# Performance work log

Hardware: AMD Instinct MI355X
Metric: run time of the kernel (lower is better)

## Reference

```python
import jax, jax.numpy as jnp
import numpy as np

N_LAYERS = 200
KSIZE = 7
L_IN = 1388
FC_IN = 188   # 1388 - 200*6
FC_OUT = 91


def setup_inputs() -> dict:
    key = jax.random.key(0)
    k_x, k_w, k_b, k_fw, k_fb = jax.random.split(key, 5)
    B = 1024
    x = jax.random.normal(k_x, (B, L_IN), dtype=jnp.float32)
    # Conv1d(1,1,7) weights: torch default init U(-s, s) with s = 1/sqrt(in_ch*k) = 1/sqrt(7)
    s = 1.0 / np.sqrt(KSIZE)
    conv_w = jax.random.uniform(k_w, (N_LAYERS, KSIZE), dtype=jnp.float32, minval=-s, maxval=s)
    conv_b = jax.random.uniform(k_b, (N_LAYERS,), dtype=jnp.float32, minval=-s, maxval=s)
    sf = 1.0 / np.sqrt(FC_IN)
    fc_w = jax.random.uniform(k_fw, (FC_OUT, FC_IN), dtype=jnp.float32, minval=-sf, maxval=sf)
    fc_b = jax.random.uniform(k_fb, (FC_OUT,), dtype=jnp.float32, minval=-sf, maxval=sf)
    return {"x": x, "conv_w": conv_w, "conv_b": conv_b, "fc_w": fc_w, "fc_b": fc_b}


def _conv1(h, w, b):
    # h: [B, L]; cross-correlation with taps w[0..6], valid padding -> [B, L-6]
    L_out = h.shape[1] - (KSIZE - 1)
    acc = w[0] * h[:, 0:L_out]
    for k in range(1, KSIZE):
        acc = acc + w[k] * h[:, k:k + L_out]
    return acc + b


def reference(x, conv_w, conv_b, fc_w, fc_b):
    h = x  # unsqueeze(1) is implicit: single channel handled as [B, L]
    for i in range(N_LAYERS):
        h = _conv1(h, conv_w[i], conv_b[i])
        if i < N_LAYERS - 1:  # last ReLU was popped in the torch module
            h = jax.nn.relu(h)
    # Linear(188, 91) applied to the length dim, then Sigmoid; squeeze channel dim
    out = jax.nn.sigmoid(h @ fc_w.T + fc_b)  # [B, 91]
    return out
```

## Files before the change

kernel.cpp:

```cpp
#include <hip/hip_runtime.h>
#include <math.h>

#define N_LAYERS 200
#define KSIZE 7
#define L_IN 1388
#define FC_IN 188
#define FC_OUT 91
#define NT 128
#define RMAX 13


template<int R, bool RELU>
__device__ __forceinline__ void run_stage(float (&r)[RMAX], float (&h)[6],
                                          const float* __restrict__ cw,
                                          const float* __restrict__ cb,
                                          int i0, int i1)
{
    constexpr int S = (R < 6) ? R : 6;
    float w[KSIZE], b;
#pragma unroll
    for (int d = 0; d < KSIZE; ++d) w[d] = cw[i0 * KSIZE + d];
    b = cb[i0];

#pragma unroll 1
    for (int i = i0; i < i1; ++i) {
#pragma unroll
        for (int k = 0; k < S; ++k) {
            float acc = b;
#pragma unroll
            for (int d = 0; d < KSIZE; ++d) {
                const int m = k + d;
                const float v = (m < R) ? r[m] : h[m - R];
                acc = fmaf(w[d], v, acc);
            }
            r[k] = RELU ? fmaxf(acc, 0.0f) : acc;
        }

        float hn[6];
#pragma unroll
        for (int t = 0; t < 6; ++t)
            hn[t] = __shfl_down(r[t % R], 1 + t / R);

        float w2[KSIZE], b2;
        const int ip = (i + 1 < i1) ? (i + 1) : i;
#pragma unroll
        for (int d = 0; d < KSIZE; ++d) w2[d] = cw[ip * KSIZE + d];
        b2 = cb[ip];

#pragma unroll
        for (int k = S; k < R; ++k) {
            float acc = b;
#pragma unroll
            for (int d = 0; d < KSIZE; ++d) {
                const int m = k + d;
                const float v = (m < R) ? r[m] : h[m - R];
                acc = fmaf(w[d], v, acc);
            }
            r[k] = RELU ? fmaxf(acc, 0.0f) : acc;
        }

#pragma unroll
        for (int t = 0; t < 6; ++t) h[t] = hn[t];
#pragma unroll
        for (int d = 0; d < KSIZE; ++d) w[d] = w2[d];
        b = b2;
    }
}

template<int Ro, int Rn>
__device__ __forceinline__ void repack(float (&r)[RMAX], float (&h)[6],
                                       float* lbuf, int lane,
                                       int base_o, int bound, int base_n)
{
#pragma unroll
    for (int k = 0; k < Ro; ++k) {
        const int g = base_o + lane * Ro + k;
        if (g < bound) lbuf[g] = r[k];
    }
    __syncthreads();
#pragma unroll
    for (int k = 0; k < Rn; ++k) r[k] = lbuf[base_n + lane * Rn + k];
#pragma unroll
    for (int t = 0; t < 6; ++t) h[t] = lbuf[base_n + lane * Rn + Rn + t];
    __syncthreads();
}

__global__ __launch_bounds__(NT) void conv_chain_kernel(
    const float* __restrict__ x,
    const float* __restrict__ conv_w,
    const float* __restrict__ conv_b,
    const float* __restrict__ fc_w,
    const float* __restrict__ fc_b,
    float* __restrict__ out)
{
    __shared__ __align__(16) float lbuf[1216];

    const int row  = blockIdx.x;
    const int tid  = threadIdx.x;
    const int lane = tid & 63;
    const int wid  = tid >> 6;

    float r[RMAX], h[6];
    const float* xr = x + (size_t)row * L_IN;
    const int base0 = wid ? 598 : 0;
#pragma unroll
    for (int k = 0; k < 13; ++k) {
        const int p = base0 + lane * 13 + k;
        r[k] = (p < L_IN) ? xr[p] : 0.0f;
    }
#pragma unroll
    for (int t = 0; t < 6; ++t) {
        const int p = base0 + lane * 13 + 13 + t;
        h[t] = (p < L_IN) ? xr[p] : 0.0f;
    }

    run_stage<13, true>(r, h, conv_w, conv_b,   0,  32);
    repack<13, 11>(r, h, lbuf, lane, wid ? 598 : 0, wid ? 1196 : 598, wid ? 502 : 0);
    run_stage<11, true>(r, h, conv_w, conv_b,  32,  64);
    repack<11, 10>(r, h, lbuf, lane, wid ? 502 : 0, wid ? 1004 : 502, wid ? 406 : 0);
    run_stage<10, true>(r, h, conv_w, conv_b,  64,  96);
    repack<10,  8>(r, h, lbuf, lane, wid ? 406 : 0, wid ?  812 : 406, wid ? 310 : 0);
    run_stage< 8, true>(r, h, conv_w, conv_b,  96, 128);
    repack< 8,  7>(r, h, lbuf, lane, wid ? 310 : 0, wid ?  620 : 310, wid ? 214 : 0);
    run_stage< 7, true>(r, h, conv_w, conv_b, 128, 160);
    repack< 7,  5>(r, h, lbuf, lane, wid ? 214 : 0, wid ?  428 : 214, wid ? 118 : 0);
    run_stage< 5, true>(r, h, conv_w, conv_b, 160, 192);
    repack< 5,  3>(r, h, lbuf, lane, wid ? 118 : 0, wid ?  236 : 118, wid ?  94 : 0);
    run_stage< 3, true >(r, h, conv_w, conv_b, 192, 199);
    run_stage< 3, false>(r, h, conv_w, conv_b, 199, 200);

    {
        const int bo = wid ? 94 : 0;
        const int bd = wid ? 188 : 94;
#pragma unroll
        for (int k = 0; k < 3; ++k) {
            const int g = bo + lane * 3 + k;
            if (g < bd) lbuf[g] = r[k];
        }
    }
    __syncthreads();

    if (tid < FC_OUT) {
        float acc = fc_b[tid];
        const float4* wp = (const float4*)(fc_w + tid * FC_IN);
        const float4* hp = (const float4*)lbuf;
#pragma unroll 4
        for (int q = 0; q < FC_IN / 4; ++q) {
            const float4 hv = hp[q];
            const float4 wv = wp[q];
            acc = fmaf(wv.x, hv.x, acc);
            acc = fmaf(wv.y, hv.y, acc);
            acc = fmaf(wv.z, hv.z, acc);
            acc = fmaf(wv.w, hv.w, acc);
        }
        out[(size_t)row * FC_OUT + tid] = 1.0f / (1.0f + expf(-acc));
    }
}

extern "C" void kernel_launch(void* const* d_in, const int* in_sizes, int n_in,
                              void* d_out, int out_size, void* d_ws, size_t ws_size,
                              hipStream_t stream) {
    const float* x      = (const float*)d_in[0];
    const float* conv_w = (const float*)d_in[1];
    const float* conv_b = (const float*)d_in[2];
    const float* fc_w   = (const float*)d_in[3];
    const float* fc_b   = (const float*)d_in[4];
    float* outp = (float*)d_out;

    const int batch = in_sizes[0] / L_IN;
    conv_chain_kernel<<<batch, NT, 0, stream>>>(x, conv_w, conv_b, fc_w, fc_b, outp);
}
```

Baseline: 135.7 us.

## Split conv chain across four waves with frequent LDS repacks

Doubles the block to four wavefronts per row, so each lane holds at most six outputs instead of thirteen. Repacking through shared memory now happens every eight layers, across 25 compile-time stages, instead of every 32. This shortens each thread's serial per-layer work and lowers register pressure, but adds many more barriers and LDS round trips, and the 1024-block grid now uses more threads per block.

```diff
diff --git a/kernel.cpp b/kernel.cpp
--- a/kernel.cpp
+++ b/kernel.cpp
@@ -6,9 +6,18 @@
 #define L_IN 1388
 #define FC_IN 188
 #define FC_OUT 91
-#define NT 128
-#define RMAX 13
+#define NT 256
+#define NW 4
+#define RMAX 6
+#define NSTAGES 25
 
+constexpr int len_end(int s) { return 1340 - 48 * s; }
+constexpr int stage_R(int s) {
+    const int l = len_end(s);
+    const int q = l / 4;
+    const int own3 = l - 3 * q;
+    return (own3 + 48 + 63) / 64;
+}
 
 template<int R, bool RELU>
 __device__ __forceinline__ void run_stage(float (&r)[RMAX], float (&h)[6],
@@ -69,21 +78,62 @@
 
 template<int Ro, int Rn>
 __device__ __forceinline__ void repack(float (&r)[RMAX], float (&h)[6],
-                                       float* lbuf, int lane,
-                                       int base_o, int bound, int base_n)
+                                       float* lbuf, int lane, int wid,
+                                       int len1, int q1, int q2)
 {
+    const int base_o = wid * q1;
+    const int bound  = (wid == 3) ? len1 : base_o + q1;
 #pragma unroll
     for (int k = 0; k < Ro; ++k) {
         const int g = base_o + lane * Ro + k;
         if (g < bound) lbuf[g] = r[k];
     }
     __syncthreads();
+    const int base_n = wid * q2;
 #pragma unroll
     for (int k = 0; k < Rn; ++k) r[k] = lbuf[base_n + lane * Rn + k];
 #pragma unroll
     for (int t = 0; t < 6; ++t) h[t] = lbuf[base_n + lane * Rn + Rn + t];
     __syncthreads();
 }
+
+template<int S>
+struct Chain {
+    __device__ static __forceinline__ void run(float (&r)[RMAX], float (&h)[6],
+        const float* __restrict__ cw, const float* __restrict__ cb,
+        float* lbuf, int lane, int wid)
+    {
+        constexpr int R = stage_R(S);
+        run_stage<R, true>(r, h, cw, cb, 8 * S, 8 * S + 8);
+        constexpr int len1 = len_end(S);
+        constexpr int q1 = len1 / 4;
+        constexpr int q2 = len_end(S + 1) / 4;
+        repack<R, stage_R(S + 1)>(r, h, lbuf, lane, wid, len1, q1, q2);
+        Chain<S + 1>::run(r, h, cw, cb, lbuf, lane, wid);
+    }
+};
+
+template<>
+struct Chain<NSTAGES - 1> {
+    __device__ static __forceinline__ void run(float (&r)[RMAX], float (&h)[6],
+        const float* __restrict__ cw, const float* __restrict__ cb,
+        float* lbuf, int lane, int wid)
+    {
+        constexpr int R = stage_R(NSTAGES - 1);
+        run_stage<R, true >(r, h, cw, cb, 8 * (NSTAGES - 1), N_LAYERS - 1);
+        run_stage<R, false>(r, h, cw, cb, N_LAYERS - 1, N_LAYERS);
+        constexpr int len1 = len_end(NSTAGES - 1);
+        constexpr int q1 = len1 / 4;
+        const int base_o = wid * q1;
+        const int bound  = (wid == 3) ? len1 : base_o + q1;
+#pragma unroll
+        for (int k = 0; k < R; ++k) {
+            const int g = base_o + lane * R + k;
+            if (g < bound) lbuf[g] = r[k];
+        }
+        __syncthreads();
+    }
+};
 
 __global__ __launch_bounds__(NT) void conv_chain_kernel(
     const float* __restrict__ x,
@@ -93,7 +143,7 @@
     const float* __restrict__ fc_b,
     float* __restrict__ out)
 {
-    __shared__ __align__(16) float lbuf[1216];
+    __shared__ __align__(16) float lbuf[1408];
 
     const int row  = blockIdx.x;
     const int tid  = threadIdx.x;
@@ -102,43 +152,20 @@
 
     float r[RMAX], h[6];
     const float* xr = x + (size_t)row * L_IN;
-    const int base0 = wid ? 598 : 0;
+    constexpr int R0 = stage_R(0);
+    const int c0 = wid * (len_end(0) / 4);
 #pragma unroll
-    for (int k = 0; k < 13; ++k) {
-        const int p = base0 + lane * 13 + k;
+    for (int k = 0; k < R0; ++k) {
+        const int p = c0 + lane * R0 + k;
         r[k] = (p < L_IN) ? xr[p] : 0.0f;
     }
 #pragma unroll
     for (int t = 0; t < 6; ++t) {
-        const int p = base0 + lane * 13 + 13 + t;
+        const int p = c0 + lane * R0 + R0 + t;
         h[t] = (p < L_IN) ? xr[p] : 0.0f;
     }
 
-    run_stage<13, true>(r, h, conv_w, conv_b,   0,  32);
-    repack<13, 11>(r, h, lbuf, lane, wid ? 598 : 0, wid ? 1196 : 598, wid ? 502 : 0);
-    run_stage<11, true>(r, h, conv_w, conv_b,  32,  64);
-    repack<11, 10>(r, h, lbuf, lane, wid ? 502 : 0, wid ? 1004 : 502, wid ? 406 : 0);
-    run_stage<10, true>(r, h, conv_w, conv_b,  64,  96);
-    repack<10,  8>(r, h, lbuf, lane, wid ? 406 : 0, wid ?  812 : 406, wid ? 310 : 0);
-    run_stage< 8, true>(r, h, conv_w, conv_b,  96, 128);
-    repack< 8,  7>(r, h, lbuf, lane, wid ? 310 : 0, wid ?  620 : 310, wid ? 214 : 0);
-    run_stage< 7, true>(r, h, conv_w, conv_b, 128, 160);
-    repack< 7,  5>(r, h, lbuf, lane, wid ? 214 : 0, wid ?  428 : 214, wid ? 118 : 0);
-    run_stage< 5, true>(r, h, conv_w, conv_b, 160, 192);
-    repack< 5,  3>(r, h, lbuf, lane, wid ? 118 : 0, wid ?  236 : 118, wid ?  94 : 0);
-    run_stage< 3, true >(r, h, conv_w, conv_b, 192, 199);
-    run_stage< 3, false>(r, h, conv_w, conv_b, 199, 200);
-
-    {
-        const int bo = wid ? 94 : 0;
-        const int bd = wid ? 188 : 94;
-#pragma unroll
-        for (int k = 0; k < 3; ++k) {
-            const int g = bo + lane * 3 + k;
-            if (g < bd) lbuf[g] = r[k];
-        }
-    }
-    __syncthreads();
+    Chain<0>::run(r, h, conv_w, conv_b, lbuf, lane, wid);
 
     if (tid < FC_OUT) {
         float acc = fc_b[tid];
```

Measured after the change: 140.8 us. 3.8% more time.
